# Optimization experiments

Hardware: AMD Instinct MI355X
Metric: run time of the kernel (lower is better)

The kernel has to match this reference:

```python
import jax, jax.numpy as jnp
import numpy as np
from jax import lax

B, L = 4, 2048
D_MODEL, D_STATE, D_CONV, EXPAND = 1024, 16, 4, 2
D_INNER = EXPAND * D_MODEL          # 2048
DT_RANK = (D_MODEL + 15) // 16      # 64 (mamba_ssm 'auto')
EPS = 1e-5


def setup_inputs() -> dict:
    key = jax.random.key(0)
    ks = jax.random.split(key, 10)
    s = 0.02
    x = jax.random.normal(ks[0], (B, L, D_MODEL), dtype=jnp.float32)
    ln_w = jnp.ones((D_MODEL,), jnp.float32)
    ln_b = jnp.zeros((D_MODEL,), jnp.float32)
    W_in = jax.random.normal(ks[1], (2 * D_INNER, D_MODEL), jnp.float32) * s
    conv_w = jax.random.normal(ks[2], (D_INNER, 1, D_CONV), jnp.float32) * s
    conv_b = jnp.zeros((D_INNER,), jnp.float32)
    W_x = jax.random.normal(ks[3], (DT_RANK + 2 * D_STATE, D_INNER), jnp.float32) * s
    W_dt = jax.random.normal(ks[4], (D_INNER, DT_RANK), jnp.float32) * s
    b_dt = jax.random.uniform(ks[5], (D_INNER,), jnp.float32, -4.0, -2.0)  # softplus(b)~small dt
    A_log = jnp.log(jnp.tile(jnp.arange(1.0, D_STATE + 1.0, dtype=jnp.float32), (D_INNER, 1)))
    Dp = jnp.ones((D_INNER,), jnp.float32)
    W_out = jax.random.normal(ks[6], (D_MODEL, D_INNER), jnp.float32) * s
    return dict(x=x, ln_w=ln_w, ln_b=ln_b, W_in=W_in, conv_w=conv_w, conv_b=conv_b,
                W_x=W_x, W_dt=W_dt, b_dt=b_dt, A_log=A_log, Dp=Dp, W_out=W_out)


def _mamba_forward(x, ln_w, ln_b, W_in, conv_w, conv_b, W_x, W_dt, b_dt, A_log, Dp, W_out):
    # LayerNorm
    mu = jnp.mean(x, axis=-1, keepdims=True)
    var = jnp.mean(jnp.square(x - mu), axis=-1, keepdims=True)
    xn = (x - mu) * lax.rsqrt(var + EPS) * ln_w + ln_b

    # in_proj -> (x_in, z), each [B, L, D_INNER]
    xz = jnp.einsum('bld,ed->ble', xn, W_in)
    x_in, z = jnp.split(xz, 2, axis=-1)

    # depthwise causal conv1d over time + SiLU
    xt = jnp.transpose(x_in, (0, 2, 1))  # [B, D_INNER, L]
    xc = lax.conv_general_dilated(xt, conv_w, window_strides=(1,),
                                  padding=[(D_CONV - 1, 0)],
                                  feature_group_count=D_INNER)
    xc = jax.nn.silu(jnp.transpose(xc + conv_b[None, :, None], (0, 2, 1)))  # [B, L, D_INNER]

    # SSM parameterization
    x_dbl = jnp.einsum('bld,ed->ble', xc, W_x)  # [B, L, DT_RANK + 2*D_STATE]
    dt_r, Bs, Cs = jnp.split(x_dbl, [DT_RANK, DT_RANK + D_STATE], axis=-1)
    dt = jax.nn.softplus(jnp.einsum('blr,dr->bld', dt_r, W_dt) + b_dt)  # [B, L, D_INNER]
    A = -jnp.exp(A_log)  # [D_INNER, D_STATE]

    # selective scan over time (time-major)
    def step(h, inp):
        dt_t, B_t, C_t, u_t = inp  # [B,dI], [B,dS], [B,dS], [B,dI]
        dA = jnp.exp(dt_t[:, :, None] * A)                     # [B, dI, dS]
        h = dA * h + (dt_t * u_t)[:, :, None] * B_t[:, None, :]
        y = jnp.sum(h * C_t[:, None, :], axis=-1)              # [B, dI]
        return h, y

    h0 = jnp.zeros((B, D_INNER, D_STATE), x.dtype)
    xs = (jnp.swapaxes(dt, 0, 1), jnp.swapaxes(Bs, 0, 1),
          jnp.swapaxes(Cs, 0, 1), jnp.swapaxes(xc, 0, 1))
    _, ys = lax.scan(step, h0, xs)
    y = jnp.swapaxes(ys, 0, 1) + xc * Dp  # [B, L, D_INNER]

    # gate + out_proj + residual
    y = y * jax.nn.silu(z)
    out = jnp.einsum('ble,de->bld', y, W_out)
    return x + out


def reference(x, ln_w, ln_b, W_in, conv_w, conv_b, W_x, W_dt, b_dt, A_log, Dp, W_out):
    return _mamba_forward(x, ln_w, ln_b, W_in, conv_w, conv_b, W_x, W_dt, b_dt, A_log, Dp, W_out)
```

## Files before the change

kernel.cpp:

```cpp
#include <hip/hip_runtime.h>
#include <math.h>

#define BB 4
#define LL 2048
#define DM 1024
#define DI 2048
#define DS 16
#define DTR 64
#define TCH 256
#define TT 16

typedef unsigned short bf16;
typedef __attribute__((ext_vector_type(8))) short bf16x8;
typedef __attribute__((ext_vector_type(4))) float f32x4;

__device__ inline float b2f(bf16 u) { return __uint_as_float(((unsigned)u) << 16); }
__device__ inline bf16 f2b(float f) {
    unsigned u = __float_as_uint(f);
    u += 0x7FFF + ((u >> 16) & 1);
    return (bf16)(u >> 16);
}

__device__ inline float4 ld4(const float* p) { return *(const float4*)p; }
__device__ inline float4 ld4(const bf16* p) {
    ushort4 v = *(const ushort4*)p;
    return make_float4(b2f(v.x), b2f(v.y), b2f(v.z), b2f(v.w));
}
__device__ inline void st1(float* p, float v) { *p = v; }
__device__ inline void st1(bf16* p, float v) { *p = f2b(v); }

__device__ inline float softplus_fast(float v) {
    return (v > 15.f) ? v : __logf(1.f + __expf(v));
}

__device__ inline void gld_lds16(const void* g, void* l) {
    __builtin_amdgcn_global_load_lds(
        (const __attribute__((address_space(1))) unsigned int*)g,
        (__attribute__((address_space(3))) unsigned int*)l, 16, 0, 0);
}

__device__ inline void dA_tree(float c1, float* dA) {
    float c2 = c1 * c1;
    float c4 = c2 * c2;
    float c8 = c4 * c4;
    dA[0]  = c1;        dA[1]  = c2;        dA[2]  = c2 * c1;
    dA[3]  = c4;        dA[4]  = c4 * c1;   dA[5]  = c4 * c2;
    dA[6]  = c4 * dA[2];dA[7]  = c8;        dA[8]  = c8 * c1;
    dA[9]  = c8 * c2;   dA[10] = c8 * dA[2];dA[11] = c8 * c4;
    dA[12] = c8 * dA[4];dA[13] = c8 * dA[5];dA[14] = c8 * dA[6];
    dA[15] = c8 * c8;
}

__global__ __launch_bounds__(256) void f2b_kernel(const float* __restrict__ in,
    bf16* __restrict__ out, int n4)
{
    int i = blockIdx.x * 256 + threadIdx.x;
    if (i >= n4) return;
    float4 v = *(const float4*)(in + (size_t)i * 4);
    ushort4 o = { f2b(v.x), f2b(v.y), f2b(v.z), f2b(v.w) };
    *(ushort4*)(out + (size_t)i * 4) = o;
}

__global__ __launch_bounds__(256) void prep_kernel(
    const float* __restrict__ x, const float* __restrict__ lw,
    const float* __restrict__ lb, bf16* __restrict__ xn,
    const float* __restrict__ W_in, bf16* __restrict__ W_in_b,
    const float* __restrict__ W_x, bf16* __restrict__ W_x_b,
    const float* __restrict__ W_dt, bf16* __restrict__ W_dt_b,
    const float* __restrict__ cw, bf16* __restrict__ cwt,
    const float* __restrict__ W_out, bf16* __restrict__ W_out_b,
    int dofast, int dowout)
{
    int blk = blockIdx.x;
    int tid = threadIdx.x;
    if (blk < BB * LL) {
        int row = blk;
        const float* xr = x + (size_t)row * DM;
        float4 v = *(const float4*)(xr + tid * 4);
        float s1 = v.x + v.y + v.z + v.w;
        float s2 = v.x * v.x + v.y * v.y + v.z * v.z + v.w * v.w;
        #pragma unroll
        for (int o = 32; o > 0; o >>= 1) {
            s1 += __shfl_xor(s1, o);
            s2 += __shfl_xor(s2, o);
        }
        __shared__ float r1[4], r2[4];
        __shared__ float smu, srs;
        int wv = tid >> 6;
        if ((tid & 63) == 0) { r1[wv] = s1; r2[wv] = s2; }
        __syncthreads();
        if (tid == 0) {
            float t1 = r1[0] + r1[1] + r1[2] + r1[3];
            float t2 = r2[0] + r2[1] + r2[2] + r2[3];
            float mu = t1 * (1.0f / DM);
            float var = t2 * (1.0f / DM) - mu * mu;
            smu = mu;
            srs = rsqrtf(var + 1e-5f);
        }
        __syncthreads();
        float mu = smu, rs = srs;
        float4 wv4 = *(const float4*)(lw + tid * 4);
        float4 bv4 = *(const float4*)(lb + tid * 4);
        ushort4 o;
        o.x = f2b((v.x - mu) * rs * wv4.x + bv4.x);
        o.y = f2b((v.y - mu) * rs * wv4.y + bv4.y);
        o.z = f2b((v.z - mu) * rs * wv4.z + bv4.z);
        o.w = f2b((v.w - mu) * rs * wv4.w + bv4.w);
        *(ushort4*)(xn + (size_t)row * DM + tid * 4) = o;
        return;
    }
    blk -= BB * LL;
    if (blk < 4096) {
        int i = blk * 256 + tid;
        float4 v = *(const float4*)(W_in + (size_t)i * 4);
        ushort4 o = { f2b(v.x), f2b(v.y), f2b(v.z), f2b(v.w) };
        *(ushort4*)(W_in_b + (size_t)i * 4) = o;
        return;
    }
    blk -= 4096;
    if (!dofast) return;
    if (blk < 192) {
        int i = blk * 256 + tid;
        float4 v = *(const float4*)(W_x + (size_t)i * 4);
        ushort4 o = { f2b(v.x), f2b(v.y), f2b(v.z), f2b(v.w) };
        *(ushort4*)(W_x_b + (size_t)i * 4) = o;
        return;
    }
    blk -= 192;
    if (blk < 128) {
        int i = blk * 256 + tid;
        float4 v = *(const float4*)(W_dt + (size_t)i * 4);
        ushort4 o = { f2b(v.x), f2b(v.y), f2b(v.z), f2b(v.w) };
        *(ushort4*)(W_dt_b + (size_t)i * 4) = o;
        return;
    }
    blk -= 128;
    if (blk < 8) {
        int d = blk * 256 + tid;
        float4 w = *(const float4*)(cw + d * 4);
        cwt[0 * DI + d] = f2b(w.x);
        cwt[1 * DI + d] = f2b(w.y);
        cwt[2 * DI + d] = f2b(w.z);
        cwt[3 * DI + d] = f2b(w.w);
        return;
    }
    blk -= 8;
    if (dowout && blk < 2048) {
        int i = blk * 256 + tid;
        float4 v = *(const float4*)(W_out + (size_t)i * 4);
        ushort4 o = { f2b(v.x), f2b(v.y), f2b(v.z), f2b(v.w) };
        *(ushort4*)(W_out_b + (size_t)i * 4) = o;
    }
}

#define BARR  do { asm volatile("" ::: "memory"); __builtin_amdgcn_s_barrier(); \
                   asm volatile("" ::: "memory"); } while (0)
#define LGKM0 do { asm volatile("s_waitcnt lgkmcnt(0)" ::: "memory"); \
                   __builtin_amdgcn_sched_barrier(0); } while (0)
#define VMC4  asm volatile("s_waitcnt vmcnt(4)" ::: "memory")
#define VMC2  asm volatile("s_waitcnt vmcnt(2)" ::: "memory")
#define SCHED0 __builtin_amdgcn_sched_barrier(0)

template<int EPI, typename TC>
__global__ __launch_bounds__(512, 2) void gemm_8p(
    const bf16* __restrict__ A, int lda,
    const bf16* __restrict__ B, int ldb,
    TC* __restrict__ C, int ldc,
    int K, const float* __restrict__ aux, int nbn)
{
    __shared__ bf16 lds[65536];
    char* L = (char*)lds;
    const int tid = threadIdx.x;
    const int lane = tid & 63;
    const int w = tid >> 6;
    const int wm = w >> 2;
    const int wn = w & 3;

    int nwg = gridDim.x;
    int bid = blockIdx.x;
    int sb = bid;
    if ((nwg & 7) == 0) sb = (bid & 7) * (nwg >> 3) + (bid >> 3);
    const int m0 = (sb / nbn) * 256;
    const int n0 = (sb % nbn) * 256;

    const size_t lda2 = (size_t)lda * 2;
    const size_t ldb2 = (size_t)ldb * 2;
    const int l8 = lane >> 3;
    const int scol = ((lane & 7) ^ l8) << 4;
    const size_t offA = (size_t)(w * 8 + l8) * lda2 + scol;
    const size_t offB = (size_t)(w * 8 + l8) * ldb2 + scol;
    const char* Ab = (const char*)A + (size_t)m0 * lda2;
    const char* Bb = (const char*)B + (size_t)n0 * ldb2;

    const int fm = lane & 15, fq = lane >> 4;
    const int prow = fm * 128;
    const int px0 = (fq << 4) ^ ((fm & 7) << 4);
    const int px1 = (64 | (fq << 4)) ^ ((fm & 7) << 4);
    const char* Lar = L + wm * 16384 + prow;
    const char* Lbr = L + 65536 + (wn >> 1) * 16384 + (wn & 1) * 8192 + prow;

    f32x4 acc[8][4] = {};
    bf16x8 a_[2][2], b_[4][2];

#define ST_A(sbuf, hh, t) do { \
    const char* s_ = Ab + (size_t)(hh) * 128 * lda2 + (size_t)(t) * 128 + offA; \
    gld_lds16(s_,             L + (sbuf) * 32768 + (hh) * 16384 + w * 1024); \
    gld_lds16(s_ + 64 * lda2, L + (sbuf) * 32768 + (hh) * 16384 + 8192 + w * 1024); \
  } while (0)
#define ST_B(sbuf, hh, t) do { \
    const char* s_ = Bb + (size_t)(hh) * 128 * ldb2 + (size_t)(t) * 128 + offB; \
    gld_lds16(s_,             L + 65536 + (sbuf) * 32768 + (hh) * 16384 + w * 1024); \
    gld_lds16(s_ + 64 * ldb2, L + 65536 + (sbuf) * 32768 + (hh) * 16384 + 8192 + w * 1024); \
  } while (0)
#define DS_A1(rb, q, kh) do { \
    a_[0][kh] = *(const bf16x8*)(Lar + (rb) * 32768 + ((q) * 32 +  0) * 128 + ((kh) ? px1 : px0)); \
    a_[1][kh] = *(const bf16x8*)(Lar + (rb) * 32768 + ((q) * 32 + 16) * 128 + ((kh) ? px1 : px0)); \
  } while (0)
#define DS_Bh(rb, kh) do { \
    _Pragma("unroll") \
    for (int ni = 0; ni < 4; ni++) \
      b_[ni][kh] = *(const bf16x8*)(Lbr + (rb) * 32768 + ni * 2048 + ((kh) ? px1 : px0)); \
  } while (0)
#define MFMA_H(q, kh) do { \
    _Pragma("unroll") \
    for (int mi = 0; mi < 2; mi++) \
      _Pragma("unroll") \
      for (int ni = 0; ni < 4; ni++) \
        acc[(q)*2+mi][ni] = __builtin_amdgcn_mfma_f32_16x16x32_bf16( \
            a_[mi][kh], b_[ni][kh], acc[(q)*2+mi][ni], 0, 0, 0); \
  } while (0)
#define PHASE(rb, q, rb2, q2, STAGE, DOVMC) do { \
    STAGE; \
    if (DOVMC) VMC4; \
    BARR; LGKM0; \
    __builtin_amdgcn_s_setprio(1); \
    MFMA_H(q, 0); \
    __builtin_amdgcn_s_setprio(0); \
    DS_A1(rb2, q2, 0); \
    if ((q) == 3) DS_Bh(rb2, 0); \
    SCHED0; \
    __builtin_amdgcn_s_setprio(1); \
    MFMA_H(q, 1); \
    __builtin_amdgcn_s_setprio(0); \
    DS_A1(rb2, q2, 1); \
    if ((q) == 3) DS_Bh(rb2, 1); \
    BARR; \
  } while (0)

    const int NT = K >> 6;
    ST_B(0, 0, 0); ST_B(0, 1, 0);
    ST_A(0, 0, 0); ST_A(0, 1, 0);
    ST_B(1, 0, 1); ST_B(1, 1, 1);
    VMC4;
    BARR;
    DS_Bh(0, 0); DS_Bh(0, 1);
    DS_A1(0, 0, 0); DS_A1(0, 0, 1);

    for (int t0 = 0; t0 < NT; t0 += 2) {
        const int tA1 = t0 + 1;
        const int tN2 = (t0 + 2 < NT) ? t0 + 2 : NT - 1;
        const int tN3 = (t0 + 3 < NT) ? t0 + 3 : NT - 1;
        PHASE(0, 0, 0, 1, ST_A(1, 0, tA1), 0);
        PHASE(0, 1, 0, 2, ST_A(1, 1, tA1), 0);
        PHASE(0, 2, 0, 3, ST_B(0, 0, tN2), 0);
        PHASE(0, 3, 1, 0, ST_B(0, 1, tN2), 1);
        PHASE(1, 0, 1, 1, ST_A(0, 0, tN2), 0);
        PHASE(1, 1, 1, 2, ST_A(0, 1, tN2), 0);
        PHASE(1, 2, 1, 3, ST_B(1, 0, tN3), 0);
        PHASE(1, 3, 0, 0, ST_B(1, 1, tN3), 1);
    }
    asm volatile("s_waitcnt vmcnt(0)" ::: "memory");

    #pragma unroll
    for (int i = 0; i < 8; i++) {
        #pragma unroll
        for (int ni = 0; ni < 4; ni++) {
            int n = n0 + wn * 64 + ni * 16 + fm;
            #pragma unroll
            for (int r = 0; r < 4; r++) {
                int m = m0 + wm * 128 + i * 16 + fq * 4 + r;
                float v = acc[i][ni][r];
                if (EPI == 2) v += aux[(size_t)m * ldc + n];
                st1(&C[(size_t)m * ldc + n], v);
            }
        }
    }
#undef ST_A
#undef ST_B
#undef DS_A1
#undef DS_Bh
#undef MFMA_H
#undef PHASE
}

template<int EPI, typename TC>
__global__ __launch_bounds__(512, 2) void gemm_8p_n128(
    const bf16* __restrict__ A, int lda,
    const bf16* __restrict__ B, int ldb,
    TC* __restrict__ C, int ldc,
    int K, const float* __restrict__ aux, int nbn)
{
    __shared__ bf16 lds[49152];
    char* L = (char*)lds;
    const int tid = threadIdx.x;
    const int lane = tid & 63;
    const int w = tid >> 6;
    const int wm = w >> 1;
    const int wn = w & 1;

    int nwg = gridDim.x;
    int bid = blockIdx.x;
    int sb = bid;
    if ((nwg & 7) == 0) sb = (bid & 7) * (nwg >> 3) + (bid >> 3);
    const int m0 = (sb / nbn) * 256;
    const int n0 = (sb % nbn) * 128;

    const size_t lda2 = (size_t)lda * 2;
    const size_t ldb2 = (size_t)ldb * 2;
    const int l8 = lane >> 3;
    const int scol = ((lane & 7) ^ l8) << 4;
    const size_t offA = (size_t)(w * 8 + l8) * lda2 + scol;
    const size_t offB = (size_t)(w * 8 + l8) * ldb2 + scol;
    const char* Ab = (const char*)A + (size_t)m0 * lda2;
    const char* Bb = (const char*)B + (size_t)n0 * ldb2;

    const int fm = lane & 15, fq = lane >> 4;
    const int prow = fm * 128;
    const int px0 = (fq << 4) ^ ((fm & 7) << 4);
    const int px1 = (64 | (fq << 4)) ^ ((fm & 7) << 4);
    const char* Lar = L + wm * 8192 + prow;
    const char* Lbr = L + 65536 + wn * 8192 + prow;

    f32x4 acc[4][4] = {};
    bf16x8 a_[2], b_[4][2];

#define ST_A(sbuf, hh, t) do { \
    const char* s_ = Ab + (size_t)(hh) * 128 * lda2 + (size_t)(t) * 128 + offA; \
    gld_lds16(s_,             L + (sbuf) * 32768 + (hh) * 16384 + w * 1024); \
    gld_lds16(s_ + 64 * lda2, L + (sbuf) * 32768 + (hh) * 16384 + 8192 + w * 1024); \
  } while (0)
#define ST_B1(sbuf, hh, t) do { \
    const char* s_ = Bb + (size_t)(hh) * 64 * ldb2 + (size_t)(t) * 128 + offB; \
    gld_lds16(s_, L + 65536 + (sbuf) * 16384 + (hh) * 8192 + w * 1024); \
  } while (0)
#define DS_A1h(rb, q, kh) do { \
    a_[kh] = *(const bf16x8*)(Lar + (rb) * 32768 + ((q) * 16) * 128 + ((kh) ? px1 : px0)); \
  } while (0)
#define DS_Bh(rb, kh) do { \
    _Pragma("unroll") \
    for (int ni = 0; ni < 4; ni++) \
      b_[ni][kh] = *(const bf16x8*)(Lbr + (rb) * 16384 + ni * 2048 + ((kh) ? px1 : px0)); \
  } while (0)
#define MFMA_Hh(q, kh) do { \
    _Pragma("unroll") \
    for (int ni = 0; ni < 4; ni++) \
      acc[q][ni] = __builtin_amdgcn_mfma_f32_16x16x32_bf16( \
          a_[kh], b_[ni][kh], acc[q][ni], 0, 0, 0); \
  } while (0)
#define PHASE(rb, q, rb2, q2, STAGE, DOVMC) do { \
    STAGE; \
    if (DOVMC) VMC2; \
    BARR; LGKM0; \
    __builtin_amdgcn_s_setprio(1); \
    MFMA_Hh(q, 0); \
    __builtin_amdgcn_s_setprio(0); \
    DS_A1h(rb2, q2, 0); \
    if ((q) == 3) DS_Bh(rb2, 0); \
    SCHED0; \
    __builtin_amdgcn_s_setprio(1); \
    MFMA_Hh(q, 1); \
    __builtin_amdgcn_s_setprio(0); \
    DS_A1h(rb2, q2, 1); \
    if ((q) == 3) DS_Bh(rb2, 1); \
    BARR; \
  } while (0)

    const int NT = K >> 6;
    ST_B1(0, 0, 0); ST_B1(0, 1, 0);
    ST_A(0, 0, 0); ST_A(0, 1, 0);
    ST_B1(1, 0, 1); ST_B1(1, 1, 1);
    VMC2;
    BARR;
    DS_Bh(0, 0); DS_Bh(0, 1);
    DS_A1h(0, 0, 0); DS_A1h(0, 0, 1);

    for (int t0 = 0; t0 < NT; t0 += 2) {
        const int tA1 = t0 + 1;
        const int tN2 = (t0 + 2 < NT) ? t0 + 2 : NT - 1;
        const int tN3 = (t0 + 3 < NT) ? t0 + 3 : NT - 1;
        PHASE(0, 0, 0, 1, ST_A(1, 0, tA1), 0);
        PHASE(0, 1, 0, 2, ST_A(1, 1, tA1), 0);
        PHASE(0, 2, 0, 3, ST_B1(0, 0, tN2), 0);
        PHASE(0, 3, 1, 0, ST_B1(0, 1, tN2), 1);
        PHASE(1, 0, 1, 1, ST_A(0, 0, tN2), 0);
        PHASE(1, 1, 1, 2, ST_A(0, 1, tN2), 0);
        PHASE(1, 2, 1, 3, ST_B1(1, 0, tN3), 0);
        PHASE(1, 3, 0, 0, ST_B1(1, 1, tN3), 1);
    }
    asm volatile("s_waitcnt vmcnt(0)" ::: "memory");

    #pragma unroll
    for (int i = 0; i < 4; i++) {
        #pragma unroll
        for (int ni = 0; ni < 4; ni++) {
            int n = n0 + wn * 64 + ni * 16 + fm;
            #pragma unroll
            for (int r = 0; r < 4; r++) {
                int m = m0 + wm * 64 + i * 16 + fq * 4 + r;
                float v = acc[i][ni][r];
                if (EPI == 2) v += aux[(size_t)m * ldc + n];
                st1(&C[(size_t)m * ldc + n], v);
            }
        }
    }
#undef ST_A
#undef ST_B1
#undef DS_A1h
#undef DS_Bh
#undef MFMA_Hh
#undef PHASE
}

template<int EPI, typename TC>
__global__ __launch_bounds__(256) void gemm_mfma(
    const bf16* __restrict__ A, int lda,
    const bf16* __restrict__ B, int ldb,
    TC* __restrict__ C, int ldc,
    int K, const float* __restrict__ aux)
{
    __shared__ bf16 As[128 * 32];
    __shared__ bf16 Bs[128 * 32];
    const int tid = threadIdx.x;
    const int lane = tid & 63;
    const int w = tid >> 6;
    const int wm = w >> 1, wn = w & 1;
    const int m0 = blockIdx.y * 128, n0 = blockIdx.x * 128;

    const int srow = lane >> 2;
    const int schunk = (lane & 3) * 8;

    const int fm = lane & 15;
    const int fq = lane >> 4;

    f32x4 acc[4][4] = {};

    for (int kt = 0; kt < K; kt += 32) {
        #pragma unroll
        for (int i = 0; i < 2; i++) {
            int r0 = i * 64 + w * 16;
            gld_lds16(A + (size_t)(m0 + r0 + srow) * lda + kt + schunk, &As[r0 * 32]);
            gld_lds16(B + (size_t)(n0 + r0 + srow) * ldb + kt + schunk, &Bs[r0 * 32]);
        }
        __syncthreads();
        bf16x8 af[4], bfr[4];
        #pragma unroll
        for (int i = 0; i < 4; i++) {
            af[i]  = *(const bf16x8*)&As[(wm * 64 + i * 16 + fm) * 32 + fq * 8];
            bfr[i] = *(const bf16x8*)&Bs[(wn * 64 + i * 16 + fm) * 32 + fq * 8];
        }
        #pragma unroll
        for (int i = 0; i < 4; i++)
            #pragma unroll
            for (int j = 0; j < 4; j++)
                acc[i][j] = __builtin_amdgcn_mfma_f32_16x16x32_bf16(
                    af[i], bfr[j], acc[i][j], 0, 0, 0);
        __syncthreads();
    }

    #pragma unroll
    for (int i = 0; i < 4; i++) {
        #pragma unroll
        for (int r = 0; r < 4; r++) {
            int m = m0 + wm * 64 + i * 16 + fq * 4 + r;
            #pragma unroll
            for (int j = 0; j < 4; j++) {
                int n = n0 + wn * 64 + j * 16 + fm;
                float v = acc[i][j][r];
                if (EPI == 1) {
                    v = softplus_fast(v + aux[n]);
                } else if (EPI == 2) {
                    v += aux[(size_t)m * ldc + n];
                }
                st1(&C[(size_t)m * ldc + n], v);
            }
        }
    }
}

__global__ __launch_bounds__(256) void xproj_mfma(
    const bf16* __restrict__ A,
    const bf16* __restrict__ Bm,
    float* __restrict__ Cx,
    bf16* __restrict__ dtr)
{
    __shared__ bf16 As[32 * 32];
    __shared__ bf16 Bs[128 * 32];
    const int tid = threadIdx.x;
    const int lane = tid & 63;
    const int w = tid >> 6;
    const int wm = w >> 1, wn = w & 1;
    const int m0 = blockIdx.x * 32;
    const int srow = lane >> 2;
    const int schunk = (lane & 3) * 8;
    const int fm = lane & 15;
    const int fq = lane >> 4;
    f32x4 acc[3] = {};
    for (int kt = 0; kt < DI; kt += 32) {
        if (w < 2) {
            int r0 = w * 16;
            gld_lds16(A + (size_t)(m0 + r0 + srow) * DI + kt + schunk, &As[r0 * 32]);
        }
        {
            int r0 = w * 32;
            gld_lds16(Bm + (size_t)(r0 + srow) * DI + kt + schunk, &Bs[r0 * 32]);
            gld_lds16(Bm + (size_t)(r0 + 16 + srow) * DI + kt + schunk, &Bs[(r0 + 16) * 32]);
        }
        __syncthreads();
        bf16x8 af = *(const bf16x8*)&As[(wm * 16 + fm) * 32 + fq * 8];
        #pragma unroll
        for (int j = 0; j < 3; j++) {
            bf16x8 bf = *(const bf16x8*)&Bs[((wn * 3 + j) * 16 + fm) * 32 + fq * 8];
            acc[j] = __builtin_amdgcn_mfma_f32_16x16x32_bf16(af, bf, acc[j], 0, 0, 0);
        }
        __syncthreads();
    }
    #pragma unroll
    for (int j = 0; j < 3; j++) {
        int col = (wn * 3 + j) * 16 + fm;
        #pragma unroll
        for (int r = 0; r < 4; r++) {
            int m = m0 + wm * 16 + fq * 4 + r;
            float v = acc[j][r];
            Cx[(size_t)m * 96 + col] = v;
            if (col < 64) dtr[(size_t)m * 64 + col] = f2b(v);
        }
    }
}

template<int EPI, typename TA, typename TB, typename TC>
__global__ __launch_bounds__(256) void gemm_nt(
    const TA* __restrict__ A, int lda,
    const TB* __restrict__ B, int ldb,
    TC* __restrict__ C, int ldc,
    int M, int N, int K,
    const float* __restrict__ aux)
{
    __shared__ float As[16][64];
    __shared__ float Bs[16][64];
    int tid = threadIdx.x;
    int m0 = blockIdx.y * 64, n0 = blockIdx.x * 64;
    int lr = tid >> 2;
    int lc = (tid & 3) * 4;
    int tm = tid >> 4;
    int tn = tid & 15;
    float acc[4][4] = {};
    for (int kt = 0; kt < K; kt += 16) {
        float4 av = ld4(A + (size_t)(m0 + lr) * lda + kt + lc);
        float4 bv = make_float4(0.f, 0.f, 0.f, 0.f);
        if (n0 + lr < N)
            bv = ld4(B + (size_t)(n0 + lr) * ldb + kt + lc);
        As[lc + 0][lr] = av.x; As[lc + 1][lr] = av.y;
        As[lc + 2][lr] = av.z; As[lc + 3][lr] = av.w;
        Bs[lc + 0][lr] = bv.x; Bs[lc + 1][lr] = bv.y;
        Bs[lc + 2][lr] = bv.z; Bs[lc + 3][lr] = bv.w;
        __syncthreads();
        #pragma unroll
        for (int k = 0; k < 16; k++) {
            float4 a4 = *(const float4*)&As[k][tm * 4];
            float4 b4 = *(const float4*)&Bs[k][tn * 4];
            float am[4] = {a4.x, a4.y, a4.z, a4.w};
            float bn[4] = {b4.x, b4.y, b4.z, b4.w};
            #pragma unroll
            for (int i = 0; i < 4; i++)
                #pragma unroll
                for (int j = 0; j < 4; j++)
                    acc[i][j] = fmaf(am[i], bn[j], acc[i][j]);
        }
        __syncthreads();
    }
    #pragma unroll
    for (int i = 0; i < 4; i++) {
        int m = m0 + tm * 4 + i;
        #pragma unroll
        for (int j = 0; j < 4; j++) {
            int n = n0 + tn * 4 + j;
            if (n >= N) continue;
            float v = acc[i][j];
            if (EPI == 1) {
                v = softplus_fast(v + aux[n]);
            }
            st1(&C[(size_t)m * ldc + n], v);
        }
    }
}

__global__ __launch_bounds__(256) void conv_silu_kernel(
    const bf16* __restrict__ xz, const bf16* __restrict__ cwt,
    const float* __restrict__ cb, bf16* __restrict__ xc)
{
    int idx = blockIdx.x * 256 + threadIdx.x;
    int d8 = idx & (DI / 8 - 1);
    int bl = idx >> 8;
    int l = bl & (LL - 1);
    int d0 = d8 * 8;
    float4 b0 = *(const float4*)(cb + d0);
    float4 b1 = *(const float4*)(cb + d0 + 4);
    float acc[8] = {b0.x, b0.y, b0.z, b0.w, b1.x, b1.y, b1.z, b1.w};
    #pragma unroll
    for (int k = 0; k < 4; k++) {
        if (l - 3 + k < 0) continue;
        bf16x8 xv = *(const bf16x8*)(xz + (size_t)(bl - 3 + k) * (2 * DI) + d0);
        bf16x8 wv = *(const bf16x8*)(cwt + k * DI + d0);
        #pragma unroll
        for (int j = 0; j < 8; j++)
            acc[j] = fmaf(b2f((bf16)xv[j]), b2f((bf16)wv[j]), acc[j]);
    }
    bf16x8 o;
    #pragma unroll
    for (int j = 0; j < 8; j++)
        o[j] = (short)f2b(acc[j] / (1.f + __expf(-acc[j])));
    *(bf16x8*)(xc + (size_t)bl * DI + d0) = o;
}

template<int NCC>
__global__ __launch_bounds__(256) void scan_part1(
    const float* __restrict__ xdbl, const bf16* __restrict__ dty,
    const bf16* __restrict__ xc, const float* __restrict__ A_log,
    float* __restrict__ P, float* __restrict__ S)
{
    __shared__ bf16 sdt[TT][TCH];
    __shared__ bf16 su[TT][TCH];
    __shared__ alignas(16) float sBC[TT][32];
    __shared__ int sflag;
    const int CH = LL / NCC;
    int bid = blockIdx.x;
    int cg = bid & 7;
    int c  = (bid >> 3) & (NCC - 1);
    int b  = (bid >> 3) / NCC;
    int d0 = cg * TCH;
    int tid = threadIdx.x;
    int w = tid >> 6, l = tid & 63;
    int lrow = l >> 5, lcol = (l & 31) * 8;
    int brow = l >> 3, bcol = (l & 7) * 4;
    int d = d0 + tid;

    if (tid == 0) sflag = 0;
    float Ads[16];
    #pragma unroll
    for (int q = 0; q < 4; q++) {
        float4 a4 = *(const float4*)&A_log[(size_t)d * DS + q * 4];
        Ads[q*4+0] = -__expf(a4.x); Ads[q*4+1] = -__expf(a4.y);
        Ads[q*4+2] = -__expf(a4.z); Ads[q*4+3] = -__expf(a4.w);
    }
    const float A0 = Ads[0];
    int bad = 0;
    #pragma unroll
    for (int s = 1; s < 16; s++) {
        float tgt = (float)(s + 1) * A0;
        bad |= (fabsf(Ads[s] - tgt) > 1e-5f * fabsf(tgt) + 1e-30f) ? 1 : 0;
    }
    __syncthreads();
    if (bad) atomicOr(&sflag, 1);
    __syncthreads();
    const int structured = (sflag == 0);

    float h[16];
    #pragma unroll
    for (int s = 0; s < 16; s++) h[s] = 0.f;
    float dsum = 0.f;

    const size_t rowbase = (size_t)b * LL + c * CH;
    for (int t0 = 0; t0 < CH; t0 += TT) {
        #pragma unroll
        for (int pp = 0; pp < 2; pp++) {
            int r0 = (pp * 4 + w) * 2;
            size_t grow = rowbase + t0 + r0 + lrow;
            gld_lds16(dty + grow * DI + d0 + lcol, &sdt[r0][0]);
            gld_lds16(xc  + grow * DI + d0 + lcol, &su[r0][0]);
        }
        if (w < 2)
            gld_lds16(xdbl + (rowbase + t0 + w * 8 + brow) * 96 + DTR + bcol,
                      &sBC[w * 8][0]);
        __syncthreads();
        for (int t = 0; t < TT; t++) {
            float dtv = b2f(sdt[t][tid]);
            float uv  = b2f(su[t][tid]);
            float tmp = dtv * uv;
            dsum += dtv;
            const float4* bc = (const float4*)&sBC[t][0];
            float4 B0 = bc[0], B1 = bc[1], B2 = bc[2], B3 = bc[3];
            float Bv[16] = {B0.x,B0.y,B0.z,B0.w, B1.x,B1.y,B1.z,B1.w,
                            B2.x,B2.y,B2.z,B2.w, B3.x,B3.y,B3.z,B3.w};
            if (structured) {
                float dA[16];
                dA_tree(__expf(dtv * A0), dA);
                #pragma unroll
                for (int s = 0; s < 16; s++)
                    h[s] = dA[s] * h[s] + tmp * Bv[s];
            } else {
                #pragma unroll
                for (int s = 0; s < 16; s++) {
                    float dA = __expf(dtv * Ads[s]);
                    h[s] = dA * h[s] + tmp * Bv[s];
                }
            }
        }
        __syncthreads();
    }
    size_t o = ((size_t)(b * NCC + c) * DI + d) * DS;
    #pragma unroll
    for (int q = 0; q < 4; q++) {
        float4 pv = make_float4(__expf(Ads[q*4+0]*dsum), __expf(Ads[q*4+1]*dsum),
                                __expf(Ads[q*4+2]*dsum), __expf(Ads[q*4+3]*dsum));
        *(float4*)&P[o + q*4] = pv;
        *(float4*)&S[o + q*4] = make_float4(h[q*4], h[q*4+1], h[q*4+2], h[q*4+3]);
    }
}

template<int NCC>
__global__ __launch_bounds__(256) void scan_combine(
    const float* __restrict__ P, float* __restrict__ S)
{
    int g = blockIdx.x * 256 + threadIdx.x;
    int b = g >> 15;
    int rem = g & 32767;
    float h = 0.f;
    #pragma unroll
    for (int c = 0; c < NCC; c++) {
        size_t o = ((size_t)(b * NCC + c) << 15) + rem;
        float p = P[o], sv = S[o];
        S[o] = h;
        h = p * h + sv;
    }
}

template<int NCC>
__global__ __launch_bounds__(256) void scan_part2(
    const float* __restrict__ xdbl, bf16* __restrict__ dty,
    const bf16* __restrict__ xc, const bf16* __restrict__ xz,
    const float* __restrict__ A_log, const float* __restrict__ Dp,
    const float* __restrict__ Hin)
{
    __shared__ bf16 sdt[TT][TCH];
    __shared__ bf16 su[TT][TCH];
    __shared__ bf16 sz[TT][TCH];
    __shared__ alignas(16) float sBC[TT][32];
    __shared__ int sflag;
    const int CH = LL / NCC;
    int bid = blockIdx.x;
    int cg = bid & 7;
    int c  = (bid >> 3) & (NCC - 1);
    int b  = (bid >> 3) / NCC;
    int d0 = cg * TCH;
    int tid = threadIdx.x;
    int w = tid >> 6, l = tid & 63;
    int lrow = l >> 5, lcol = (l & 31) * 8;
    int brow = l >> 3, bcol = (l & 7) * 4;
    int d = d0 + tid;

    if (tid == 0) sflag = 0;
    float Ads[16];
    #pragma unroll
    for (int q = 0; q < 4; q++) {
        float4 a4 = *(const float4*)&A_log[(size_t)d * DS + q * 4];
        Ads[q*4+0] = -__expf(a4.x); Ads[q*4+1] = -__expf(a4.y);
        Ads[q*4+2] = -__expf(a4.z); Ads[q*4+3] = -__expf(a4.w);
    }
    const float A0 = Ads[0];
    int bad = 0;
    #pragma unroll
    for (int s = 1; s < 16; s++) {
        float tgt = (float)(s + 1) * A0;
        bad |= (fabsf(Ads[s] - tgt) > 1e-5f * fabsf(tgt) + 1e-30f) ? 1 : 0;
    }
    __syncthreads();
    if (bad) atomicOr(&sflag, 1);
    __syncthreads();
    const int structured = (sflag == 0);

    float h[16];
    size_t ho = ((size_t)(b * NCC + c) * DI + d) * DS;
    #pragma unroll
    for (int q = 0; q < 4; q++) {
        float4 hv = *(const float4*)&Hin[ho + q*4];
        h[q*4] = hv.x; h[q*4+1] = hv.y; h[q*4+2] = hv.z; h[q*4+3] = hv.w;
    }
    float dpd = Dp[d];

    const size_t rowbase = (size_t)b * LL + c * CH;
    for (int t0 = 0; t0 < CH; t0 += TT) {
        #pragma unroll
        for (int pp = 0; pp < 2; pp++) {
            int r0 = (pp * 4 + w) * 2;
            size_t grow = rowbase + t0 + r0 + lrow;
            gld_lds16(dty + grow * DI + d0 + lcol, &sdt[r0][0]);
            gld_lds16(xc  + grow * DI + d0 + lcol, &su[r0][0]);
            gld_lds16(xz  + grow * (2 * DI) + DI + d0 + lcol, &sz[r0][0]);
        }
        if (w < 2)
            gld_lds16(xdbl + (rowbase + t0 + w * 8 + brow) * 96 + DTR + bcol,
                      &sBC[w * 8][0]);
        __syncthreads();
        for (int t = 0; t < TT; t++) {
            float dtv = b2f(sdt[t][tid]);
            float uv  = b2f(su[t][tid]);
            float tmp = dtv * uv;
            const float4* bc = (const float4*)&sBC[t][0];
            float4 B0 = bc[0], B1 = bc[1], B2 = bc[2], B3 = bc[3];
            float4 C0 = bc[4], C1 = bc[5], C2 = bc[6], C3 = bc[7];
            float Bv[16] = {B0.x,B0.y,B0.z,B0.w, B1.x,B1.y,B1.z,B1.w,
                            B2.x,B2.y,B2.z,B2.w, B3.x,B3.y,B3.z,B3.w};
            float Cv[16] = {C0.x,C0.y,C0.z,C0.w, C1.x,C1.y,C1.z,C1.w,
                            C2.x,C2.y,C2.z,C2.w, C3.x,C3.y,C3.z,C3.w};
            float y0 = 0.f, y1 = 0.f;
            if (structured) {
                float dA[16];
                dA_tree(__expf(dtv * A0), dA);
                #pragma unroll
                for (int s = 0; s < 16; s++) {
                    h[s] = dA[s] * h[s] + tmp * Bv[s];
                    if (s & 1) y1 = fmaf(h[s], Cv[s], y1);
                    else       y0 = fmaf(h[s], Cv[s], y0);
                }
            } else {
                #pragma unroll
                for (int s = 0; s < 16; s++) {
                    float dA = __expf(dtv * Ads[s]);
                    h[s] = dA * h[s] + tmp * Bv[s];
                    if (s & 1) y1 = fmaf(h[s], Cv[s], y1);
                    else       y0 = fmaf(h[s], Cv[s], y0);
                }
            }
            float y = y0 + y1;
            float zv = b2f(sz[t][tid]);
            float yo = (y + uv * dpd) * (zv / (1.f + __expf(-zv)));
            dty[(rowbase + t0 + t) * DI + d] = f2b(yo);
        }
        __syncthreads();
    }
}

__global__ __launch_bounds__(256) void scan_mono(
    const float* __restrict__ xdbl, bf16* __restrict__ dty,
    const bf16* __restrict__ xc, const bf16* __restrict__ xz,
    const float* __restrict__ A_log, const float* __restrict__ Dp)
{
    const int TC = 64;
    int b = blockIdx.x >> 7;
    int dblk = blockIdx.x & 127;
    int d0 = dblk * 16;
    int tid = threadIdx.x;
    int s = tid & 15;
    int dg = tid >> 4;
    int d = d0 + dg;
    float Ads = -__expf(A_log[(size_t)d * DS + s]);
    float h = 0.f;
    __shared__ float sdt[TC][16], su[TC][16], sB[TC][16], sC[TC][16], sy[TC][16];
    const size_t rowbase = (size_t)b * LL;
    int wi = tid >> 2;
    int wj = (tid & 3) * 4;
    float4 dpv = *(const float4*)(Dp + d0 + wj);
    for (int t0 = 0; t0 < LL; t0 += TC) {
        {
            size_t g = (rowbase + t0 + wi) * (size_t)DI + d0 + wj;
            *(float4*)&sdt[wi][wj] = ld4(dty + g);
            *(float4*)&su[wi][wj]  = ld4(xc + g);
        }
        #pragma unroll
        for (int r = 0; r < 4; r++) {
            int i = (tid >> 4) + r * 16;
            size_t g = (rowbase + t0 + i) * 96;
            sB[i][s] = xdbl[g + DTR + s];
            sC[i][s] = xdbl[g + DTR + DS + s];
        }
        __syncthreads();
        for (int i = 0; i < TC; i++) {
            float dtv = sdt[i][dg];
            float dA = __expf(dtv * Ads);
            h = dA * h + dtv * su[i][dg] * sB[i][s];
            float yp = h * sC[i][s];
            yp += __shfl_xor(yp, 1);
            yp += __shfl_xor(yp, 2);
            yp += __shfl_xor(yp, 4);
            yp += __shfl_xor(yp, 8);
            if (s == 0) sy[i][dg] = yp;
        }
        __syncthreads();
        {
            size_t g  = (rowbase + t0 + wi) * (size_t)DI + d0 + wj;
            size_t gz = (rowbase + t0 + wi) * (size_t)(2 * DI) + DI + d0 + wj;
            float4 zv = ld4(xz + gz);
            float4 yv = *(const float4*)&sy[wi][wj];
            float4 uv = *(const float4*)&su[wi][wj];
            ushort4 o;
            o.x = f2b((yv.x + uv.x * dpv.x) * (zv.x / (1.f + __expf(-zv.x))));
            o.y = f2b((yv.y + uv.y * dpv.y) * (zv.y / (1.f + __expf(-zv.y))));
            o.z = f2b((yv.z + uv.z * dpv.z) * (zv.z / (1.f + __expf(-zv.z))));
            o.w = f2b((yv.w + uv.w * dpv.w) * (zv.w / (1.f + __expf(-zv.w))));
            *(ushort4*)(dty + g) = o;
        }
        __syncthreads();
    }
}

__global__ __launch_bounds__(256) void conv_silu_slow(
    const bf16* __restrict__ xz, const float* __restrict__ cw,
    const float* __restrict__ cb, bf16* __restrict__ xc)
{
    int idx = blockIdx.x * 256 + threadIdx.x;
    int d4 = idx & (DI / 4 - 1);
    int bl = idx >> 9;
    int l = bl & (LL - 1);
    int d0 = d4 * 4;
    float4 bias = *(const float4*)(cb + d0);
    float acc[4] = {bias.x, bias.y, bias.z, bias.w};
    #pragma unroll
    for (int k = 0; k < 4; k++) {
        if (l - 3 + k < 0) continue;
        float4 xv = ld4(xz + (size_t)(bl - 3 + k) * (2 * DI) + d0);
        acc[0] = fmaf(xv.x, cw[(d0 + 0) * 4 + k], acc[0]);
        acc[1] = fmaf(xv.y, cw[(d0 + 1) * 4 + k], acc[1]);
        acc[2] = fmaf(xv.z, cw[(d0 + 2) * 4 + k], acc[2]);
        acc[3] = fmaf(xv.w, cw[(d0 + 3) * 4 + k], acc[3]);
    }
    ushort4 o;
    o.x = f2b(acc[0] / (1.f + __expf(-acc[0])));
    o.y = f2b(acc[1] / (1.f + __expf(-acc[1])));
    o.z = f2b(acc[2] / (1.f + __expf(-acc[2])));
    o.w = f2b(acc[3] / (1.f + __expf(-acc[3])));
    *(ushort4*)(xc + (size_t)bl * DI + d0) = o;
}

extern "C" void kernel_launch(void* const* d_in, const int* in_sizes, int n_in,
                              void* d_out, int out_size, void* d_ws, size_t ws_size,
                              hipStream_t stream)
{
    const float* x      = (const float*)d_in[0];
    const float* ln_w   = (const float*)d_in[1];
    const float* ln_b   = (const float*)d_in[2];
    const float* W_in   = (const float*)d_in[3];
    const float* conv_w = (const float*)d_in[4];
    const float* conv_b = (const float*)d_in[5];
    const float* W_x    = (const float*)d_in[6];
    const float* W_dt   = (const float*)d_in[7];
    const float* b_dt   = (const float*)d_in[8];
    const float* A_log  = (const float*)d_in[9];
    const float* Dp     = (const float*)d_in[10];
    const float* W_out  = (const float*)d_in[11];
    float* out = (float*)d_out;

    const size_t R = (size_t)BB * LL;

    bf16*  xz    = (bf16*)d_ws;
    bf16*  dty   = xz + R * 2 * DI;
    float* xdbl  = (float*)(dty + R * DI);
    float* Pbuf  = xdbl + R * 96;

    const size_t headB = (size_t)((char*)Pbuf - (char*)d_ws);
    const size_t tailB = (size_t)(128 * DI + DI * DTR + R * DTR + 4 * DI) * 2 + 64;
    const size_t ps32B = (size_t)BB * 32 * DI * DS * 4;
    const size_t ps16B = (size_t)BB * 16 * DI * DS * 4;
    const int ncc = (ws_size >= headB + 2 * ps32B + tailB) ? 32 : 16;
    const size_t psB = (ncc == 32) ? ps32B : ps16B;

    float* Sbuf   = (float*)((char*)Pbuf + psB);
    bf16*  W_x_b  = (bf16*)((char*)Sbuf + psB);
    bf16*  W_dt_b = W_x_b + 128 * DI;
    bf16*  dtr    = W_dt_b + DI * DTR;
    bf16*  cwt    = dtr + R * DTR;
    bf16*  W_out_b2 = cwt + 4 * DI;
    const size_t ws_need = (size_t)((char*)(cwt + 4 * DI) - (char*)d_ws);
    const bool fast = ws_size >= ws_need;
    const size_t ws_need_w = (size_t)((char*)(W_out_b2 + (size_t)DM * DI) - (char*)d_ws);
    const int dowout = (fast && ws_size >= ws_need_w) ? 1 : 0;

    bf16*  W_in_b  = dty;
    bf16*  W_out_b = xz;

    bf16* xn = (bf16*)d_out;
    bf16* xc = (bf16*)d_out;

    {
        int nb = BB * LL + 4096;
        if (fast) nb += 192 + 128 + 8 + (dowout ? 2048 : 0);
        prep_kernel<<<nb, 256, 0, stream>>>(
            x, ln_w, ln_b, xn, W_in, W_in_b, W_x, W_x_b, W_dt, W_dt_b,
            conv_w, cwt, W_out, W_out_b2, fast ? 1 : 0, dowout);
    }

    for (int half = 0; half < 2; half++) {
        gemm_8p<0, bf16><<<dim3(16 * 16), 512, 0, stream>>>(
            xn + (size_t)half * 4096 * DM, DM, W_in_b, DM,
            xz + (size_t)half * 4096 * (2 * DI), 2 * DI, DM, nullptr, 16);
    }

    if (fast) {
        conv_silu_kernel<<<(int)(R * DI / 8 / 256), 256, 0, stream>>>(
            xz, cwt, conv_b, xc);
        xproj_mfma<<<(int)(R / 32), 256, 0, stream>>>(xc, W_x_b, xdbl, dtr);
        gemm_mfma<1, bf16><<<dim3(DI / 128, R / 128), 256, 0, stream>>>(
            dtr, DTR, W_dt_b, DTR, dty, DI, DTR, b_dt);
        if (ncc == 32) {
            scan_part1<32><<<BB * 32 * (DI / TCH), 256, 0, stream>>>(
                xdbl, dty, xc, A_log, Pbuf, Sbuf);
            scan_combine<32><<<BB * DI * DS / 256, 256, 0, stream>>>(Pbuf, Sbuf);
            scan_part2<32><<<BB * 32 * (DI / TCH), 256, 0, stream>>>(
                xdbl, dty, xc, xz, A_log, Dp, Sbuf);
        } else {
            scan_part1<16><<<BB * 16 * (DI / TCH), 256, 0, stream>>>(
                xdbl, dty, xc, A_log, Pbuf, Sbuf);
            scan_combine<16><<<BB * DI * DS / 256, 256, 0, stream>>>(Pbuf, Sbuf);
            scan_part2<16><<<BB * 16 * (DI / TCH), 256, 0, stream>>>(
                xdbl, dty, xc, xz, A_log, Dp, Sbuf);
        }
    } else {
        conv_silu_slow<<<(int)(R * DI / 4 / 256), 256, 0, stream>>>(
            xz, conv_w, conv_b, xc);
        gemm_nt<0><<<dim3(2, R / 64), 256, 0, stream>>>(
            xc, DI, W_x, DI, xdbl, 96, (int)R, 96, DI, nullptr);
        gemm_nt<1><<<dim3(DI / 64, R / 64), 256, 0, stream>>>(
            xdbl, 96, W_dt, DTR, dty, DI, (int)R, DI, DTR, b_dt);
        scan_mono<<<BB * (DI / 16), 256, 0, stream>>>(
            xdbl, dty, xc, xz, A_log, Dp);
    }

    const bf16* W_out_use = dowout ? (const bf16*)W_out_b2 : (const bf16*)W_out_b;
    if (!dowout)
        f2b_kernel<<<(DM * DI / 4) / 256, 256, 0, stream>>>(W_out, W_out_b, DM * DI / 4);

    gemm_8p_n128<2, float><<<dim3((int)(R / 256) * (DM / 128)), 512, 0, stream>>>(
        dty, DI, W_out_use, DI, out, DM, DI, x, DM / 128);
}
```

Before: 400.0 us.

## Load scan inputs directly from global and add 64-chunk scan split

The scan kernels no longer stage dt, u and z tiles through LDS with async global-to-LDS copies. Each thread now reads its own column straight from global memory inside an unrolled time loop, which saves LDS capacity and staging instructions. Separately, the host picks 64 time chunks when the workspace is large enough, giving more blocks for parallelism at the cost of larger P/S buffers and more combine work. The direct loads are 2-byte per-thread accesses, coalesced across the block but narrower than the previous 16-byte staging loads.

Measured after the change: 433.6 us. 1.08x slower.

```diff
diff --git a/kernel.cpp b/kernel.cpp
--- a/kernel.cpp
+++ b/kernel.cpp
@@ -628,8 +628,6 @@
     const bf16* __restrict__ xc, const float* __restrict__ A_log,
     float* __restrict__ P, float* __restrict__ S)
 {
-    __shared__ bf16 sdt[TT][TCH];
-    __shared__ bf16 su[TT][TCH];
     __shared__ alignas(16) float sBC[TT][32];
     __shared__ int sflag;
     const int CH = LL / NCC;
@@ -640,7 +638,6 @@
     int d0 = cg * TCH;
     int tid = threadIdx.x;
     int w = tid >> 6, l = tid & 63;
-    int lrow = l >> 5, lcol = (l & 31) * 8;
     int brow = l >> 3, bcol = (l & 7) * 4;
     int d = d0 + tid;
 
@@ -671,20 +668,15 @@
 
     const size_t rowbase = (size_t)b * LL + c * CH;
     for (int t0 = 0; t0 < CH; t0 += TT) {
-        #pragma unroll
-        for (int pp = 0; pp < 2; pp++) {
-            int r0 = (pp * 4 + w) * 2;
-            size_t grow = rowbase + t0 + r0 + lrow;
-            gld_lds16(dty + grow * DI + d0 + lcol, &sdt[r0][0]);
-            gld_lds16(xc  + grow * DI + d0 + lcol, &su[r0][0]);
-        }
         if (w < 2)
             gld_lds16(xdbl + (rowbase + t0 + w * 8 + brow) * 96 + DTR + bcol,
                       &sBC[w * 8][0]);
         __syncthreads();
+        #pragma unroll
         for (int t = 0; t < TT; t++) {
-            float dtv = b2f(sdt[t][tid]);
-            float uv  = b2f(su[t][tid]);
+            size_t g = (rowbase + t0 + t) * DI + d;
+            float dtv = b2f(dty[g]);
+            float uv  = b2f(xc[g]);
             float tmp = dtv * uv;
             dsum += dtv;
             const float4* bc = (const float4*)&sBC[t][0];
@@ -741,9 +733,6 @@
     const float* __restrict__ A_log, const float* __restrict__ Dp,
     const float* __restrict__ Hin)
 {
-    __shared__ bf16 sdt[TT][TCH];
-    __shared__ bf16 su[TT][TCH];
-    __shared__ bf16 sz[TT][TCH];
     __shared__ alignas(16) float sBC[TT][32];
     __shared__ int sflag;
     const int CH = LL / NCC;
@@ -754,7 +743,6 @@
     int d0 = cg * TCH;
     int tid = threadIdx.x;
     int w = tid >> 6, l = tid & 63;
-    int lrow = l >> 5, lcol = (l & 31) * 8;
     int brow = l >> 3, bcol = (l & 7) * 4;
     int d = d0 + tid;
 
@@ -789,21 +777,16 @@
 
     const size_t rowbase = (size_t)b * LL + c * CH;
     for (int t0 = 0; t0 < CH; t0 += TT) {
-        #pragma unroll
-        for (int pp = 0; pp < 2; pp++) {
-            int r0 = (pp * 4 + w) * 2;
-            size_t grow = rowbase + t0 + r0 + lrow;
-            gld_lds16(dty + grow * DI + d0 + lcol, &sdt[r0][0]);
-            gld_lds16(xc  + grow * DI + d0 + lcol, &su[r0][0]);
-            gld_lds16(xz  + grow * (2 * DI) + DI + d0 + lcol, &sz[r0][0]);
-        }
         if (w < 2)
             gld_lds16(xdbl + (rowbase + t0 + w * 8 + brow) * 96 + DTR + bcol,
                       &sBC[w * 8][0]);
         __syncthreads();
+        #pragma unroll
         for (int t = 0; t < TT; t++) {
-            float dtv = b2f(sdt[t][tid]);
-            float uv  = b2f(su[t][tid]);
+            size_t g = (rowbase + t0 + t) * DI + d;
+            float dtv = b2f(dty[g]);
+            float uv  = b2f(xc[g]);
+            float zv  = b2f(xz[(rowbase + t0 + t) * (2 * DI) + DI + d]);
             float tmp = dtv * uv;
             const float4* bc = (const float4*)&sBC[t][0];
             float4 B0 = bc[0], B1 = bc[1], B2 = bc[2], B3 = bc[3];
@@ -832,9 +815,8 @@
                 }
             }
             float y = y0 + y1;
-            float zv = b2f(sz[t][tid]);
             float yo = (y + uv * dpd) * (zv / (1.f + __expf(-zv)));
-            dty[(rowbase + t0 + t) * DI + d] = f2b(yo);
+            dty[g] = f2b(yo);
         }
         __syncthreads();
     }
@@ -958,10 +940,11 @@
 
     const size_t headB = (size_t)((char*)Pbuf - (char*)d_ws);
     const size_t tailB = (size_t)(128 * DI + DI * DTR + R * DTR + 4 * DI) * 2 + 64;
-    const size_t ps32B = (size_t)BB * 32 * DI * DS * 4;
-    const size_t ps16B = (size_t)BB * 16 * DI * DS * 4;
-    const int ncc = (ws_size >= headB + 2 * ps32B + tailB) ? 32 : 16;
-    const size_t psB = (ncc == 32) ? ps32B : ps16B;
+    const size_t psU   = (size_t)BB * DI * DS * 4;
+    int ncc = 16;
+    if (ws_size >= headB + 2 * (64 * psU) + tailB) ncc = 64;
+    else if (ws_size >= headB + 2 * (32 * psU) + tailB) ncc = 32;
+    const size_t psB = (size_t)ncc * psU;
 
     float* Sbuf   = (float*)((char*)Pbuf + psB);
     bf16*  W_x_b  = (bf16*)((char*)Sbuf + psB);
@@ -1000,7 +983,13 @@
         xproj_mfma<<<(int)(R / 32), 256, 0, stream>>>(xc, W_x_b, xdbl, dtr);
         gemm_mfma<1, bf16><<<dim3(DI / 128, R / 128), 256, 0, stream>>>(
             dtr, DTR, W_dt_b, DTR, dty, DI, DTR, b_dt);
-        if (ncc == 32) {
+        if (ncc == 64) {
+            scan_part1<64><<<BB * 64 * (DI / TCH), 256, 0, stream>>>(
+                xdbl, dty, xc, A_log, Pbuf, Sbuf);
+            scan_combine<64><<<BB * DI * DS / 256, 256, 0, stream>>>(Pbuf, Sbuf);
+            scan_part2<64><<<BB * 64 * (DI / TCH), 256, 0, stream>>>(
+                xdbl, dty, xc, xz, A_log, Dp, Sbuf);
+        } else if (ncc == 32) {
             scan_part1<32><<<BB * 32 * (DI / TCH), 256, 0, stream>>>(
                 xdbl, dty, xc, A_log, Pbuf, Sbuf);
             scan_combine<32><<<BB * DI * DS / 256, 256, 0, stream>>>(Pbuf, Sbuf);
```
